# Kernel tuning notes

Measured on AMD Instinct MI355X. Metric: run time of the kernel, lower is better.

The kernel has to match this reference:

```python
import jax, jax.numpy as jnp
import numpy as np

# Dimensions: B batches, E links, T time steps, F flows, rank-r factors, K unrolled iters
B, E, T, F = 16, 256, 4096, 512
RANK = 10
NUM_ITER = 5


def setup_inputs() -> dict:
    key = jax.random.key(0)
    ks = jax.random.split(key, 9)
    Y = jax.random.normal(ks[0], (B, E, T), dtype=jnp.float32)
    R = (jax.random.uniform(ks[1], (B, E, F)) < 0.1).astype(jnp.float32)
    Omega = (jax.random.uniform(ks[2], (B, E, T)) < 0.9).astype(jnp.float32)
    P0 = jax.random.normal(ks[3], (B, E, RANK), dtype=jnp.float32) * 0.1
    Q0 = jax.random.normal(ks[4], (B, T, RANK), dtype=jnp.float32) * 0.1
    # per-iteration learned log-parameters of the unrolled network
    lam_log = jax.random.normal(ks[5], (NUM_ITER,), dtype=jnp.float32) * 0.1 - 1.0
    mu_log = jax.random.normal(ks[6], (NUM_ITER,), dtype=jnp.float32) * 0.1 - 1.0
    nu_log = jax.random.normal(ks[7], (NUM_ITER,), dtype=jnp.float32) * 0.1
    gamma_logit = jax.random.normal(ks[8], (NUM_ITER,), dtype=jnp.float32) * 0.1
    return {"Y": Y, "R": R, "Omega": Omega, "P0": P0, "Q0": Q0,
            "lam_log": lam_log, "mu_log": mu_log, "nu_log": nu_log,
            "gamma_logit": gamma_logit}


def reference(Y, R, Omega, P0, Q0, lam_log, mu_log, nu_log, gamma_logit):
    """Unrolled BSCA: Y ~ X + R @ A + noise on observed entries (Omega mask),
    X relaxed low-rank via factors P (B,E,r), Q (B,T,r); A sparse anomalies (B,F,T).
    Each iteration: rank-r ridge solves for P and Q (left=False -> rhs @ inv(lhs)),
    relaxed X update, soft-thresholded BSCA direction for A + convex-combination step."""
    rank = P0.shape[-1]
    eye = jnp.eye(rank, dtype=Y.dtype)
    X = Omega * Y                     # (B,E,T) init relaxed variable
    A = jnp.zeros((*Y.shape[:-2], R.shape[-1], Y.shape[-1]), dtype=Y.dtype)  # (B,F,T)
    P, Q = P0, Q0
    A_scale = (R * R).mT @ (Omega * Omega)          # (B,F,T)
    noobs = A_scale == 0
    A_scale_safe = A_scale + noobs.astype(Y.dtype)
    for k in range(NUM_ITER):
        lam = jnp.exp(lam_log[k])
        mu = jnp.exp(mu_log[k])
        nu = jnp.exp(nu_log[k])
        gamma = jax.nn.sigmoid(gamma_logit[k])
        regp = lam / nu
        # P update: P = (X @ Q) @ inv(Q^T Q + regp I)   (right solve; lhs symmetric)
        lhsQ = Q.mT @ Q + regp * eye                 # (B,r,r)
        P = jnp.linalg.solve(lhsQ, (X @ Q).mT).mT    # (B,E,r)
        # Q update: Q = (X^T @ P) @ inv(P^T P + regp I)
        lhsP = P.mT @ P + regp * eye
        Q = jnp.linalg.solve(lhsP, (X.mT @ P).mT).mT # (B,T,r)
        # X update (relaxed): X = (Omega*err + nu*P Q^T) / (Omega^2 + nu)
        RA = R @ A                                   # (B,E,T)
        err = Omega * (Y - RA)
        X = (Omega * err + nu * (P @ Q.mT)) / (Omega * Omega + nu)
        # A update: soft-thresholded best-response + convex combination step
        resid = Omega * (Y - X - RA)                 # (B,E,T)
        BA = A + (R.mT @ resid) / A_scale_safe       # (B,F,T)
        A_dir = jnp.sign(BA) * jnp.maximum(jnp.abs(BA) - mu / A_scale_safe, 0.0)
        A_dir = jnp.where(noobs, 0.0, A_dir)
        A = A + gamma * (A_dir - A)
    return A
```

## Files before the change

### kernel.cpp

```cpp
#include <hip/hip_runtime.h>
#include <stdint.h>

#define BB 16
#define EE 256
#define TT 4096
#define FF 512
#define RK 10
#define NIT 5

typedef short bf16x8 __attribute__((ext_vector_type(8)));
typedef float f32x4  __attribute__((ext_vector_type(4)));

__device__ __forceinline__ unsigned short f2bf(float x){
  unsigned int u = __float_as_uint(x);
  unsigned int r = (u + 0x7FFFu + ((u >> 16) & 1u)) >> 16;
  return (unsigned short)r;
}
__device__ __forceinline__ float bf2f(unsigned short s){
  return __uint_as_float(((unsigned int)s) << 16);
}

__device__ __forceinline__ void gld16(const void* g, void* l){
  __builtin_amdgcn_global_load_lds((const __attribute__((address_space(1))) unsigned int*)g,
                                   (__attribute__((address_space(3))) unsigned int*)l,
                                   16, 0, 0);
}

__device__ __forceinline__ int ssw(int r, int s){
  return ((s ^ (r & 3) ^ ((r >> 2) & 3)) << 3);
}


__global__ void k_params(const float* lam_log, const float* mu_log,
                         const float* nu_log, const float* gl, float* prm){
  int k = threadIdx.x;
  if (k < NIT){
    float lam = expf(lam_log[k]);
    float mu  = expf(mu_log[k]);
    float nu  = expf(nu_log[k]);
    float gam = 1.0f/(1.0f+expf(-gl[k]));
    prm[k*8+0]=lam; prm[k*8+1]=mu; prm[k*8+2]=nu; prm[k*8+3]=gam; prm[k*8+4]=lam/nu;
  }
}

__global__ void k_initX(const float4* __restrict__ Y, const float4* __restrict__ Om,
                        float4* __restrict__ X, ushort4* __restrict__ Omb){
  int i = blockIdx.x*256 + threadIdx.x;
  float4 y = Y[i], o = Om[i];
  X[i] = make_float4(y.x*o.x, y.y*o.y, y.z*o.z, y.w*o.w);
  ushort4 ob; ob.x=f2bf(o.x); ob.y=f2bf(o.y); ob.z=f2bf(o.z); ob.w=f2bf(o.w);
  Omb[i] = ob;
}

__global__ void k_qtrans(const float* __restrict__ Q0, float* __restrict__ Qt){
  int idx = blockIdx.x*256 + threadIdx.x;
  int b = idx >> 12, t = idx & (TT-1);
  #pragma unroll
  for (int j=0;j<RK;j++)
    Qt[((size_t)b*RK + j)*TT + t] = Q0[(size_t)idx*RK + j];
}

__global__ void k_rbf(const float4* __restrict__ R, ushort4* __restrict__ Rb){
  int i = blockIdx.x*256 + threadIdx.x;
  float4 v = R[i];
  ushort4 o; o.x=f2bf(v.x); o.y=f2bf(v.y); o.z=f2bf(v.z); o.w=f2bf(v.w);
  Rb[i] = o;
}

__global__ void k_rtransb(const float* __restrict__ Rm, unsigned short* __restrict__ Rbt){
  int f = blockIdx.x, b = blockIdx.y, e = threadIdx.x;
  Rbt[((size_t)b*FF + f)*EE + e] = f2bf(Rm[((size_t)b*EE + e)*FF + f]);
}

__global__ void k_omtrans(const unsigned short* __restrict__ Omb,
                          unsigned short* __restrict__ OmbT){
  __shared__ unsigned short sT[64][66];
  int b  = blockIdx.z;
  int E0 = blockIdx.y*64, T0 = blockIdx.x*64;
  int tid = threadIdx.x;
  int fi = tid >> 4;
  int m  = tid & 15;
  #pragma unroll
  for (int pass=0; pass<4; ++pass){
    int e = pass*16 + fi;
    ushort4 v = *(const ushort4*)(Omb + ((size_t)(b*EE + E0 + e))*TT + T0 + m*4);
    sT[e][m*4+0]=v.x; sT[e][m*4+1]=v.y; sT[e][m*4+2]=v.z; sT[e][m*4+3]=v.w;
  }
  __syncthreads();
  #pragma unroll
  for (int pass=0; pass<4; ++pass){
    int t  = pass*16 + fi;
    int e4 = m*4;
    ushort4 o;
    o.x = sT[e4+0][t]; o.y = sT[e4+1][t];
    o.z = sT[e4+2][t]; o.w = sT[e4+3][t];
    *(ushort4*)(OmbT + ((size_t)b*TT + T0 + t)*EE + E0 + e4) = o;
  }
}


__global__ void k_lhsQ(const float* __restrict__ Qt, const float* __restrict__ prm,
                       float* __restrict__ lhs, int k){
  int p = blockIdx.x, b = blockIdx.y;
  int i = 0, rem = p;
  while (rem >= i+1){ rem -= (i+1); ++i; }
  int j = rem;
  const float* qi = Qt + ((size_t)b*RK + i)*TT;
  const float* qj = Qt + ((size_t)b*RK + j)*TT;
  float a = 0.0f;
  for (int t = threadIdx.x*4; t < TT; t += 1024){
    float4 x = *(const float4*)(qi+t);
    float4 y = *(const float4*)(qj+t);
    a += x.x*y.x + x.y*y.y + x.z*y.z + x.w*y.w;
  }
  __shared__ float red[256];
  red[threadIdx.x] = a; __syncthreads();
  for (int s=128; s>0; s>>=1){
    if (threadIdx.x < s) red[threadIdx.x] += red[threadIdx.x+s];
    __syncthreads();
  }
  if (threadIdx.x==0){
    float v = red[0];
    if (i==j) v += prm[k*8+4];
    lhs[(b*RK+i)*RK + j] = v;
    lhs[(b*RK+j)*RK + i] = v;
  }
}

__global__ void k_lhsP(const float* __restrict__ P, const float* __restrict__ prm,
                       float* __restrict__ lhs, int k){
  int p = blockIdx.x, b = blockIdx.y;
  int i = 0, rem = p;
  while (rem >= i+1){ rem -= (i+1); ++i; }
  int j = rem;
  int e = threadIdx.x;
  const float* pr = P + ((size_t)b*EE + e)*RK;
  float a = pr[i]*pr[j];
  __shared__ float red[256];
  red[threadIdx.x] = a; __syncthreads();
  for (int s=128; s>0; s>>=1){
    if (threadIdx.x < s) red[threadIdx.x] += red[threadIdx.x+s];
    __syncthreads();
  }
  if (threadIdx.x==0){
    float v = red[0];
    if (i==j) v += prm[k*8+4];
    lhs[(b*RK+i)*RK + j] = v;
    lhs[(b*RK+j)*RK + i] = v;
  }
}

__global__ void k_invert(const float* __restrict__ lhs, float* __restrict__ inv){
  int b = blockIdx.x;
  __shared__ float aug[RK][2*RK];
  int tid = threadIdx.x;
  int i = tid / (2*RK), j = tid % (2*RK);
  bool act = tid < RK*2*RK;
  if (act) aug[i][j] = (j < RK) ? lhs[(b*RK+i)*RK + j] : ((j-RK)==i ? 1.0f : 0.0f);
  __syncthreads();
  for (int kk=0; kk<RK; ++kk){
    float pinv = 1.0f / aug[kk][kk];
    __syncthreads();
    if (act && i==kk) aug[i][j] *= pinv;
    __syncthreads();
    float factor = (act && i!=kk) ? aug[i][kk] : 0.0f;
    float pivrow = act ? aug[kk][j] : 0.0f;
    __syncthreads();
    if (act && i!=kk) aug[i][j] -= factor * pivrow;
    __syncthreads();
  }
  if (act && j >= RK) inv[(b*RK+i)*RK + (j-RK)] = aug[i][j];
}

__global__ void k_Pupd(const float* __restrict__ X, const float* __restrict__ Qt,
                       const float* __restrict__ inv, float* __restrict__ P){
  int e = blockIdx.x, b = blockIdx.y;
  const float* xr = X + ((size_t)b*EE + e)*TT;
  const float* qb = Qt + (size_t)b*RK*TT;
  float acc[RK];
  #pragma unroll
  for (int j=0;j<RK;j++) acc[j]=0.0f;
  for (int t = threadIdx.x*4; t < TT; t += 1024){
    float4 x = *(const float4*)(xr+t);
    #pragma unroll
    for (int j=0;j<RK;j++){
      float4 q = *(const float4*)(qb + (size_t)j*TT + t);
      acc[j] += x.x*q.x + x.y*q.y + x.z*q.z + x.w*q.w;
    }
  }
  __shared__ float partial[4][RK];
  int lane = threadIdx.x & 63, wv = threadIdx.x >> 6;
  #pragma unroll
  for (int j=0;j<RK;j++){
    float v = acc[j];
    for (int s=32;s>0;s>>=1) v += __shfl_down(v, s, 64);
    if (lane==0) partial[wv][j] = v;
  }
  __syncthreads();
  if (threadIdx.x < RK){
    int i = threadIdx.x;
    float out = 0.0f;
    #pragma unroll
    for (int j=0;j<RK;j++){
      float xq = partial[0][j]+partial[1][j]+partial[2][j]+partial[3][j];
      out += xq * inv[(b*RK+j)*RK + i];
    }
    P[((size_t)b*EE + e)*RK + i] = out;
  }
}

__global__ void k_Qupd(const float* __restrict__ X, const float* __restrict__ P,
                       const float* __restrict__ inv, float* __restrict__ Qt){
  int b = blockIdx.y;
  int t = blockIdx.x*256 + threadIdx.x;
  __shared__ float sP[EE*RK];
  __shared__ float sInv[RK*RK];
  for (int i=threadIdx.x; i<EE*RK; i+=256) sP[i] = P[(size_t)b*EE*RK + i];
  if (threadIdx.x < RK*RK) sInv[threadIdx.x] = inv[b*RK*RK + threadIdx.x];
  __syncthreads();
  float acc[RK];
  #pragma unroll
  for (int j=0;j<RK;j++) acc[j]=0.0f;
  const float* xb = X + (size_t)b*EE*TT + t;
  for (int e=0;e<EE;e++){
    float x = xb[(size_t)e*TT];
    #pragma unroll
    for (int j=0;j<RK;j++) acc[j] += x * sP[e*RK+j];
  }
  #pragma unroll
  for (int i=0;i<RK;i++){
    float q = 0.0f;
    #pragma unroll
    for (int j=0;j<RK;j++) q += acc[j]*sInv[j*RK+i];
    Qt[((size_t)b*RK + i)*TT + t] = q;
  }
}

__global__ __launch_bounds__(256) void k_gemm1m(
    const unsigned short* __restrict__ Abt, const unsigned short* __restrict__ Rb,
    const float* __restrict__ Y, const unsigned short* __restrict__ Omb,
    const float* __restrict__ Qt, const float* __restrict__ P,
    const float* __restrict__ prm, float* __restrict__ X,
    unsigned short* __restrict__ residT, int k)
{
  __shared__ __align__(16) unsigned char lds[20480];
  int id = blockIdx.x;
  int b  = id >> 6;
  int e0 = ((id >> 5) & 1) * 128;
  int t0 = (id & 31) * 128;
  int tid  = threadIdx.x;
  int lane = tid & 63, wid = tid >> 6;
  int lr = lane & 15, lg = lane >> 4;
  int wm = wid >> 1, wn = wid & 1;

  f32x4 acc[4][4];
  #pragma unroll
  for (int m=0;m<4;++m)
    #pragma unroll
    for (int n=0;n<4;++n)
      #pragma unroll
      for (int i=0;i<4;++i) acc[m][n][i]=0.0f;

  if (k > 0){
    int swz  = ((lg ^ (lr & 3) ^ ((lr >> 2) & 3)) << 4);
    int aoff = (wm*64 + lr)*64 + swz;
    int boff = 8192 + (wn*64 + lr)*64 + swz;
    int c0 = tid, c1 = tid + 256;
    int r0 = c0 >> 2, s0 = c0 & 3;
    int r1 = c1 >> 2, s1 = c1 & 3;
    const unsigned short* gA0 = Abt + ((size_t)b*TT + t0 + r0)*FF + ssw(r0,s0);
    const unsigned short* gA1 = Abt + ((size_t)b*TT + t0 + r1)*FF + ssw(r1,s1);
    const unsigned short* gB0 = Rb  + ((size_t)(b*EE + e0 + r0))*FF + ssw(r0,s0);
    const unsigned short* gB1 = Rb  + ((size_t)(b*EE + e0 + r1))*FF + ssw(r1,s1);
    unsigned char* lA0 = lds + c0*16;
    unsigned char* lA1 = lds + c1*16;
    unsigned char* lB0 = lds + 8192 + c0*16;
    unsigned char* lB1 = lds + 8192 + c1*16;

    for (int kk=0; kk<16; ++kk){
      __syncthreads();
      int f0k = kk*32;
      gld16(gA0 + f0k, lA0);
      gld16(gA1 + f0k, lA1);
      gld16(gB0 + f0k, lB0);
      gld16(gB1 + f0k, lB1);
      asm volatile("s_waitcnt vmcnt(0)" ::: "memory");
      __syncthreads();
      bf16x8 af[4], bb[4];
      #pragma unroll
      for (int m=0;m<4;++m) af[m] = *(const bf16x8*)(lds + aoff + m*1024);
      #pragma unroll
      for (int n=0;n<4;++n) bb[n] = *(const bf16x8*)(lds + boff + n*1024);
      #pragma unroll
      for (int m=0;m<4;++m)
        #pragma unroll
        for (int n=0;n<4;++n)
          acc[m][n] = __builtin_amdgcn_mfma_f32_16x16x32_bf16(af[m], bb[n], acc[m][n], 0, 0, 0);
    }
  }

  __syncthreads();
  unsigned short* wbuf = (unsigned short*)(lds + wid*2176);
  float* Pl = (float*)(lds + 8704);
  float* Ql = (float*)(lds + 8704 + 5120);
  for (int idx = tid; idx < 128*RK; idx += 256)
    Pl[idx] = P[((size_t)(b*EE + e0))*RK + idx];
  for (int idx = tid; idx < RK*128; idx += 256){
    int j = idx >> 7, t = idx & 127;
    Ql[idx] = Qt[((size_t)(b*RK + j))*TT + t0 + t];
  }
  __syncthreads();

  float nu = prm[k*8+2];
  #pragma unroll
  for (int m=0;m<4;++m){
    int tq = wm*64 + m*16 + lg*4;
    float4 ql4[RK];
    #pragma unroll
    for (int j=0;j<RK;++j) ql4[j] = *(const float4*)(Ql + j*128 + tq);
    asm volatile("" ::: "memory");
    #pragma unroll
    for (int n=0;n<4;++n){
      int eloc = wn*64 + n*16 + lr;
      const float* pr = Pl + eloc*RK;
      float4 pq = {0,0,0,0};
      #pragma unroll
      for (int j=0;j<RK;++j){
        float pj = pr[j];
        pq.x += pj*ql4[j].x; pq.y += pj*ql4[j].y;
        pq.z += pj*ql4[j].z; pq.w += pj*ql4[j].w;
      }
      f32x4 ra = acc[m][n];
      size_t off = ((size_t)(b*EE + e0 + eloc))*TT + t0 + tq;
      float4 y = *(const float4*)(Y + off);
      ushort4 ou = *(const ushort4*)(Omb + off);
      float4 xo; float rs0, rs1, rs2, rs3;
      {
        float o = bf2f(ou.x), om2 = o*o, d = y.x - ra[0];
        xo.x = (om2*d + nu*pq.x)/(om2 + nu); rs0 = o*(y.x - xo.x - ra[0]);
      }{
        float o = bf2f(ou.y), om2 = o*o, d = y.y - ra[1];
        xo.y = (om2*d + nu*pq.y)/(om2 + nu); rs1 = o*(y.y - xo.y - ra[1]);
      }{
        float o = bf2f(ou.z), om2 = o*o, d = y.z - ra[2];
        xo.z = (om2*d + nu*pq.z)/(om2 + nu); rs2 = o*(y.z - xo.z - ra[2]);
      }{
        float o = bf2f(ou.w), om2 = o*o, d = y.w - ra[3];
        xo.w = (om2*d + nu*pq.w)/(om2 + nu); rs3 = o*(y.w - xo.w - ra[3]);
      }
      *(float4*)(X + off) = xo;
      int wc = n*16 + lr;
      wbuf[(lg*4+0)*68 + wc] = f2bf(rs0);
      wbuf[(lg*4+1)*68 + wc] = f2bf(rs1);
      wbuf[(lg*4+2)*68 + wc] = f2bf(rs2);
      wbuf[(lg*4+3)*68 + wc] = f2bf(rs3);
    }
    asm volatile("" ::: "memory");
    #pragma unroll
    for (int j2=0;j2<4;++j2){
      int row = j2*4 + lg;
      int c4  = lr*4;
      ushort4 vv = *(const ushort4*)(wbuf + row*68 + c4);
      *(ushort4*)(residT + ((size_t)b*TT + t0 + wm*64 + m*16 + row)*EE + e0 + wn*64 + c4) = vv;
    }
    asm volatile("" ::: "memory");
  }
}

__device__ __forceinline__ float aupd(float a, float g, unsigned short asu,
                                      float mu, float gamma){
  float as = bf2f(asu);
  bool no = (as == 0.0f);
  float rs = 1.0f / (no ? 1.0f : as);
  float ba = a + g*rs;
  float ad = copysignf(fmaxf(fabsf(ba) - mu*rs, 0.0f), ba);
  if (no) ad = 0.0f;
  return a + gamma*(ad - a);
}

__global__ __launch_bounds__(256) void k_gemm2m(
    const unsigned short* __restrict__ residT, const unsigned short* __restrict__ Rbt,
    const unsigned short* __restrict__ As, const float* __restrict__ prm,
    float* __restrict__ A, unsigned short* __restrict__ Abt, int k)
{
  __shared__ __align__(16) unsigned char lds[16384];
  int id = blockIdx.x;
  int b  = id >> 7;
  int f0 = ((id >> 5) & 3) * 128;
  int t0 = (id & 31) * 128;
  int tid  = threadIdx.x;
  int lane = tid & 63, wid = tid >> 6;
  int lr = lane & 15, lg = lane >> 4;
  int wm = wid >> 1, wn = wid & 1;

  f32x4 acc[4][4];
  #pragma unroll
  for (int m=0;m<4;++m)
    #pragma unroll
    for (int n=0;n<4;++n)
      #pragma unroll
      for (int i=0;i<4;++i) acc[m][n][i]=0.0f;

  int swz  = ((lg ^ (lr & 3) ^ ((lr >> 2) & 3)) << 4);
  int aoff = (wm*64 + lr)*64 + swz;
  int boff = 8192 + (wn*64 + lr)*64 + swz;
  int c0 = tid, c1 = tid + 256;
  int r0 = c0 >> 2, s0 = c0 & 3;
  int r1 = c1 >> 2, s1 = c1 & 3;
  const unsigned short* gA0 = residT + ((size_t)b*TT + t0 + r0)*EE + ssw(r0,s0);
  const unsigned short* gA1 = residT + ((size_t)b*TT + t0 + r1)*EE + ssw(r1,s1);
  const unsigned short* gB0 = Rbt    + ((size_t)(b*FF + f0 + r0))*EE + ssw(r0,s0);
  const unsigned short* gB1 = Rbt    + ((size_t)(b*FF + f0 + r1))*EE + ssw(r1,s1);
  unsigned char* lA0 = lds + c0*16;
  unsigned char* lA1 = lds + c1*16;
  unsigned char* lB0 = lds + 8192 + c0*16;
  unsigned char* lB1 = lds + 8192 + c1*16;

  for (int kk=0; kk<8; ++kk){
    __syncthreads();
    int eoff = kk*32;
    gld16(gA0 + eoff, lA0);
    gld16(gA1 + eoff, lA1);
    gld16(gB0 + eoff, lB0);
    gld16(gB1 + eoff, lB1);
    asm volatile("s_waitcnt vmcnt(0)" ::: "memory");
    __syncthreads();
    bf16x8 af[4], bb[4];
    #pragma unroll
    for (int m=0;m<4;++m) af[m] = *(const bf16x8*)(lds + aoff + m*1024);
    #pragma unroll
    for (int n=0;n<4;++n) bb[n] = *(const bf16x8*)(lds + boff + n*1024);
    #pragma unroll
    for (int m=0;m<4;++m)
      #pragma unroll
      for (int n=0;n<4;++n)
        acc[m][n] = __builtin_amdgcn_mfma_f32_16x16x32_bf16(af[m], bb[n], acc[m][n], 0, 0, 0);
  }

  __syncthreads();
  unsigned short* wbuf = (unsigned short*)(lds + wid*2176);
  float mu = prm[k*8+1], gamma = prm[k*8+3];
  bool emit = (k < NIT-1);
  #pragma unroll
  for (int m=0;m<4;++m){
    int tq = wm*64 + m*16 + lg*4;
    #pragma unroll
    for (int n=0;n<4;++n){
      int floc = wn*64 + n*16 + lr;
      size_t off = ((size_t)(b*FF + f0 + floc))*TT + t0 + tq;
      float4 a = *(const float4*)(A + off);
      ushort4 as4 = *(const ushort4*)(As + off);
      f32x4 g = acc[m][n];
      float4 an;
      an.x = aupd(a.x, g[0], as4.x, mu, gamma);
      an.y = aupd(a.y, g[1], as4.y, mu, gamma);
      an.z = aupd(a.z, g[2], as4.z, mu, gamma);
      an.w = aupd(a.w, g[3], as4.w, mu, gamma);
      *(float4*)(A + off) = an;
      if (emit){
        int wc = n*16 + lr;
        wbuf[(lg*4+0)*68 + wc] = f2bf(an.x);
        wbuf[(lg*4+1)*68 + wc] = f2bf(an.y);
        wbuf[(lg*4+2)*68 + wc] = f2bf(an.z);
        wbuf[(lg*4+3)*68 + wc] = f2bf(an.w);
      }
    }
    asm volatile("" ::: "memory");
    if (emit){
      #pragma unroll
      for (int j2=0;j2<4;++j2){
        int row = j2*4 + lg;
        int c4  = lr*4;
        ushort4 vv = *(const ushort4*)(wbuf + row*68 + c4);
        *(ushort4*)(Abt + ((size_t)b*TT + t0 + wm*64 + m*16 + row)*FF + f0 + wn*64 + c4) = vv;
      }
    }
    asm volatile("" ::: "memory");
  }
}

__global__ __launch_bounds__(256) void k_ascalem(
    const unsigned short* __restrict__ OmbT, const unsigned short* __restrict__ Rbt,
    unsigned short* __restrict__ As)
{
  __shared__ __align__(16) unsigned char lds[16384];
  int id = blockIdx.x;
  int b  = id >> 7;
  int f0 = ((id >> 5) & 3) * 128;
  int t0 = (id & 31) * 128;
  int tid  = threadIdx.x;
  int lane = tid & 63, wid = tid >> 6;
  int lr = lane & 15, lg = lane >> 4;
  int wm = wid >> 1, wn = wid & 1;

  f32x4 acc[4][4];
  #pragma unroll
  for (int m=0;m<4;++m)
    #pragma unroll
    for (int n=0;n<4;++n)
      #pragma unroll
      for (int i=0;i<4;++i) acc[m][n][i]=0.0f;

  int swz  = ((lg ^ (lr & 3) ^ ((lr >> 2) & 3)) << 4);
  int aoff = (wm*64 + lr)*64 + swz;
  int boff = 8192 + (wn*64 + lr)*64 + swz;
  int c0 = tid, c1 = tid + 256;
  int r0 = c0 >> 2, s0 = c0 & 3;
  int r1 = c1 >> 2, s1 = c1 & 3;
  const unsigned short* gA0 = OmbT + ((size_t)b*TT + t0 + r0)*EE + ssw(r0,s0);
  const unsigned short* gA1 = OmbT + ((size_t)b*TT + t0 + r1)*EE + ssw(r1,s1);
  const unsigned short* gB0 = Rbt  + ((size_t)(b*FF + f0 + r0))*EE + ssw(r0,s0);
  const unsigned short* gB1 = Rbt  + ((size_t)(b*FF + f0 + r1))*EE + ssw(r1,s1);
  unsigned char* lA0 = lds + c0*16;
  unsigned char* lA1 = lds + c1*16;
  unsigned char* lB0 = lds + 8192 + c0*16;
  unsigned char* lB1 = lds + 8192 + c1*16;

  for (int kk=0; kk<8; ++kk){
    __syncthreads();
    int eoff = kk*32;
    gld16(gA0 + eoff, lA0);
    gld16(gA1 + eoff, lA1);
    gld16(gB0 + eoff, lB0);
    gld16(gB1 + eoff, lB1);
    asm volatile("s_waitcnt vmcnt(0)" ::: "memory");
    __syncthreads();
    bf16x8 af[4], bb[4];
    #pragma unroll
    for (int m=0;m<4;++m) af[m] = *(const bf16x8*)(lds + aoff + m*1024);
    #pragma unroll
    for (int n=0;n<4;++n) bb[n] = *(const bf16x8*)(lds + boff + n*1024);
    #pragma unroll
    for (int m=0;m<4;++m)
      #pragma unroll
      for (int n=0;n<4;++n)
        acc[m][n] = __builtin_amdgcn_mfma_f32_16x16x32_bf16(af[m], bb[n], acc[m][n], 0, 0, 0);
  }

  #pragma unroll
  for (int m=0;m<4;++m){
    int tq = wm*64 + m*16 + lg*4;
    #pragma unroll
    for (int n=0;n<4;++n){
      int floc = wn*64 + n*16 + lr;
      size_t off = ((size_t)(b*FF + f0 + floc))*TT + t0 + tq;
      ushort4 o;
      o.x = f2bf(acc[m][n][0]); o.y = f2bf(acc[m][n][1]);
      o.z = f2bf(acc[m][n][2]); o.w = f2bf(acc[m][n][3]);
      *(ushort4*)(As + off) = o;
    }
  }
}


extern "C" void kernel_launch(void* const* d_in, const int* in_sizes, int n_in,
                              void* d_out, int out_size, void* d_ws, size_t ws_size,
                              hipStream_t stream){
  const float* Y   = (const float*)d_in[0];
  const float* Rm  = (const float*)d_in[1];
  const float* Om  = (const float*)d_in[2];
  const float* P0  = (const float*)d_in[3];
  const float* Q0  = (const float*)d_in[4];
  const float* lam = (const float*)d_in[5];
  const float* mu  = (const float*)d_in[6];
  const float* nu  = (const float*)d_in[7];
  const float* gl  = (const float*)d_in[8];
  float* A = (float*)d_out;

  char* ws = (char*)d_ws;
  const size_t X_OFF    = 0;
  const size_t REST_OFF = X_OFF    + (size_t)BB*EE*TT*4;
  const size_t OMB_OFF  = REST_OFF + (size_t)BB*TT*EE*2;
  const size_t AS_OFF   = OMB_OFF  + (size_t)BB*EE*TT*2;
  const size_t QT_OFF   = AS_OFF   + (size_t)BB*FF*TT*2;
  const size_t P_OFF    = QT_OFF   + (size_t)BB*RK*TT*4;
  const size_t LHS_OFF  = P_OFF    + (size_t)BB*EE*RK*4;
  const size_t INV_OFF  = LHS_OFF  + (size_t)BB*RK*RK*4;
  const size_t PRM_OFF  = INV_OFF  + (size_t)BB*RK*RK*4;
  const size_t RB_OFF   = PRM_OFF  + 4096;
  const size_t RBT_OFF  = RB_OFF   + (size_t)BB*EE*FF*2;
  const size_t OMBT_OFF = RBT_OFF  + (size_t)BB*FF*EE*2;
  const size_t ABT_OFF  = OMBT_OFF + (size_t)BB*TT*EE*2;

  float* X    = (float*)(ws + X_OFF);
  unsigned short* residT = (unsigned short*)(ws + REST_OFF);
  unsigned short* Omb    = (unsigned short*)(ws + OMB_OFF);
  unsigned short* As     = (unsigned short*)(ws + AS_OFF);
  float* Qt   = (float*)(ws + QT_OFF);
  float* P    = (float*)(ws + P_OFF);
  float* lhs  = (float*)(ws + LHS_OFF);
  float* inv  = (float*)(ws + INV_OFF);
  float* prm  = (float*)(ws + PRM_OFF);
  unsigned short* Rb   = (unsigned short*)(ws + RB_OFF);
  unsigned short* Rbt  = (unsigned short*)(ws + RBT_OFF);
  unsigned short* OmbT = (unsigned short*)(ws + OMBT_OFF);
  unsigned short* Abt  = (unsigned short*)(ws + ABT_OFF);

  (void)P0; (void)Om; (void)in_sizes; (void)n_in; (void)ws_size;

  hipMemsetAsync(d_out, 0, (size_t)out_size*sizeof(float), stream);
  k_params<<<1, 64, 0, stream>>>(lam, mu, nu, gl, prm);
  k_initX<<<BB*EE*TT/4/256, 256, 0, stream>>>((const float4*)Y, (const float4*)Om,
                                              (float4*)X, (ushort4*)Omb);
  k_qtrans<<<BB*TT/256, 256, 0, stream>>>(Q0, Qt);
  k_rbf<<<BB*EE*FF/4/256, 256, 0, stream>>>((const float4*)Rm, (ushort4*)Rb);
  k_rtransb<<<dim3(FF, BB), 256, 0, stream>>>(Rm, Rbt);
  k_omtrans<<<dim3(TT/64, EE/64, BB), 256, 0, stream>>>(Omb, OmbT);
  k_ascalem<<<2048, 256, 0, stream>>>(OmbT, Rbt, As);

  for (int k=0; k<NIT; ++k){
    k_lhsQ  <<<dim3(55, BB), 256, 0, stream>>>(Qt, prm, lhs, k);
    k_invert<<<BB, 256, 0, stream>>>(lhs, inv);
    k_Pupd  <<<dim3(EE, BB), 256, 0, stream>>>(X, Qt, inv, P);
    k_lhsP  <<<dim3(55, BB), 256, 0, stream>>>(P, prm, lhs, k);
    k_invert<<<BB, 256, 0, stream>>>(lhs, inv);
    k_Qupd  <<<dim3(TT/256, BB), 256, 0, stream>>>(X, P, inv, Qt);
    k_gemm1m<<<BB*2*32, 256, 0, stream>>>(Abt, Rb, Y, Omb, Qt, P, prm, X, residT, k);
    k_gemm2m<<<2048, 256, 0, stream>>>(residT, Rbt, As, prm, A, Abt, k);
  }
}
```

Measured before the change: 1.797 ms.

## Halve GEMM tile sizes for more blocks and pack Omega into bitmask

The two per-iteration MFMA GEMM kernels get smaller output tiles: gemm1m goes to 64x128 and 2048 blocks, gemm2m to 128x64 and 4096 blocks. This raises block count and lowers per-block registers and LDS to improve occupancy and load balance across CUs. Separately, a new kernel packs the binary Omega mask into 32-bit bitmasks with wave ballots, so gemm1m reads one bit per element instead of a bf16 value. The bitmask relies on Omega being binary. Smaller tiles mean more redundant operand loads per output.

```diff
diff --git a/kernel.cpp b/kernel.cpp
--- a/kernel.cpp
+++ b/kernel.cpp
@@ -50,6 +50,18 @@
   X[i] = make_float4(y.x*o.x, y.y*o.y, y.z*o.z, y.w*o.w);
   ushort4 ob; ob.x=f2bf(o.x); ob.y=f2bf(o.y); ob.z=f2bf(o.z); ob.w=f2bf(o.w);
   Omb[i] = ob;
+}
+
+__global__ void k_ombit(const float* __restrict__ Om, unsigned int* __restrict__ Ombit){
+  int tid = threadIdx.x;
+  int wv = tid >> 6, lane = tid & 63;
+  size_t base = (size_t)blockIdx.x*8192 + (size_t)wv*2048;
+  for (int it=0; it<32; ++it){
+    float om = Om[base + it*64 + lane];
+    unsigned long long m = __ballot(om != 0.0f);
+    if (lane==0)  Ombit[(base>>5) + it*2]     = (unsigned int)m;
+    if (lane==32) Ombit[(base>>5) + it*2 + 1] = (unsigned int)(m>>32);
+  }
 }
 
 __global__ void k_qtrans(const float* __restrict__ Q0, float* __restrict__ Qt){
@@ -238,24 +250,24 @@
 
 __global__ __launch_bounds__(256) void k_gemm1m(
     const unsigned short* __restrict__ Abt, const unsigned short* __restrict__ Rb,
-    const float* __restrict__ Y, const unsigned short* __restrict__ Omb,
+    const float* __restrict__ Y, const unsigned int* __restrict__ Ombit,
     const float* __restrict__ Qt, const float* __restrict__ P,
     const float* __restrict__ prm, float* __restrict__ X,
     unsigned short* __restrict__ residT, int k)
 {
   __shared__ __align__(16) unsigned char lds[20480];
   int id = blockIdx.x;
-  int b  = id >> 6;
-  int e0 = ((id >> 5) & 1) * 128;
-  int t0 = (id & 31) * 128;
+  int b  = id >> 7;
+  int e0 = ((id >> 6) & 1) * 128;
+  int t0 = (id & 63) * 64;
   int tid  = threadIdx.x;
   int lane = tid & 63, wid = tid >> 6;
   int lr = lane & 15, lg = lane >> 4;
   int wm = wid >> 1, wn = wid & 1;
 
-  f32x4 acc[4][4];
-  #pragma unroll
-  for (int m=0;m<4;++m)
+  f32x4 acc[2][4];
+  #pragma unroll
+  for (int m=0;m<2;++m)
     #pragma unroll
     for (int n=0;n<4;++n)
       #pragma unroll
@@ -263,36 +275,34 @@
 
   if (k > 0){
     int swz  = ((lg ^ (lr & 3) ^ ((lr >> 2) & 3)) << 4);
-    int aoff = (wm*64 + lr)*64 + swz;
-    int boff = 8192 + (wn*64 + lr)*64 + swz;
+    int aoff = (wm*32 + lr)*64 + swz;
+    int boff = 4096 + (wn*64 + lr)*64 + swz;
+    int rA = tid >> 2, sA = tid & 3;
     int c0 = tid, c1 = tid + 256;
-    int r0 = c0 >> 2, s0 = c0 & 3;
-    int r1 = c1 >> 2, s1 = c1 & 3;
-    const unsigned short* gA0 = Abt + ((size_t)b*TT + t0 + r0)*FF + ssw(r0,s0);
-    const unsigned short* gA1 = Abt + ((size_t)b*TT + t0 + r1)*FF + ssw(r1,s1);
-    const unsigned short* gB0 = Rb  + ((size_t)(b*EE + e0 + r0))*FF + ssw(r0,s0);
-    const unsigned short* gB1 = Rb  + ((size_t)(b*EE + e0 + r1))*FF + ssw(r1,s1);
-    unsigned char* lA0 = lds + c0*16;
-    unsigned char* lA1 = lds + c1*16;
-    unsigned char* lB0 = lds + 8192 + c0*16;
-    unsigned char* lB1 = lds + 8192 + c1*16;
+    int rB0 = c0 >> 2, sB0 = c0 & 3;
+    int rB1 = c1 >> 2, sB1 = c1 & 3;
+    const unsigned short* gA  = Abt + ((size_t)b*TT + t0 + rA)*FF + ssw(rA,sA);
+    const unsigned short* gB0 = Rb  + ((size_t)(b*EE + e0 + rB0))*FF + ssw(rB0,sB0);
+    const unsigned short* gB1 = Rb  + ((size_t)(b*EE + e0 + rB1))*FF + ssw(rB1,sB1);
+    unsigned char* lA  = lds + tid*16;
+    unsigned char* lB0 = lds + 4096 + c0*16;
+    unsigned char* lB1 = lds + 4096 + c1*16;
 
     for (int kk=0; kk<16; ++kk){
       __syncthreads();
       int f0k = kk*32;
-      gld16(gA0 + f0k, lA0);
-      gld16(gA1 + f0k, lA1);
+      gld16(gA  + f0k, lA);
       gld16(gB0 + f0k, lB0);
       gld16(gB1 + f0k, lB1);
       asm volatile("s_waitcnt vmcnt(0)" ::: "memory");
       __syncthreads();
-      bf16x8 af[4], bb[4];
-      #pragma unroll
-      for (int m=0;m<4;++m) af[m] = *(const bf16x8*)(lds + aoff + m*1024);
+      bf16x8 af[2], bb[4];
+      #pragma unroll
+      for (int m=0;m<2;++m) af[m] = *(const bf16x8*)(lds + aoff + m*1024);
       #pragma unroll
       for (int n=0;n<4;++n) bb[n] = *(const bf16x8*)(lds + boff + n*1024);
       #pragma unroll
-      for (int m=0;m<4;++m)
+      for (int m=0;m<2;++m)
         #pragma unroll
         for (int n=0;n<4;++n)
           acc[m][n] = __builtin_amdgcn_mfma_f32_16x16x32_bf16(af[m], bb[n], acc[m][n], 0, 0, 0);
@@ -301,23 +311,23 @@
 
   __syncthreads();
   unsigned short* wbuf = (unsigned short*)(lds + wid*2176);
-  float* Pl = (float*)(lds + 8704);
-  float* Ql = (float*)(lds + 8704 + 5120);
+  float* Pl = (float*)(lds + 12288);
+  float* Ql = (float*)(lds + 12288 + 5120);
   for (int idx = tid; idx < 128*RK; idx += 256)
     Pl[idx] = P[((size_t)(b*EE + e0))*RK + idx];
-  for (int idx = tid; idx < RK*128; idx += 256){
-    int j = idx >> 7, t = idx & 127;
+  for (int idx = tid; idx < RK*64; idx += 256){
+    int j = idx >> 6, t = idx & 63;
     Ql[idx] = Qt[((size_t)(b*RK + j))*TT + t0 + t];
   }
   __syncthreads();
 
   float nu = prm[k*8+2];
   #pragma unroll
-  for (int m=0;m<4;++m){
-    int tq = wm*64 + m*16 + lg*4;
+  for (int m=0;m<2;++m){
+    int tq = wm*32 + m*16 + lg*4;
     float4 ql4[RK];
     #pragma unroll
-    for (int j=0;j<RK;++j) ql4[j] = *(const float4*)(Ql + j*128 + tq);
+    for (int j=0;j<RK;++j) ql4[j] = *(const float4*)(Ql + j*64 + tq);
     asm volatile("" ::: "memory");
     #pragma unroll
     for (int n=0;n<4;++n){
@@ -333,20 +343,21 @@
       f32x4 ra = acc[m][n];
       size_t off = ((size_t)(b*EE + e0 + eloc))*TT + t0 + tq;
       float4 y = *(const float4*)(Y + off);
-      ushort4 ou = *(const ushort4*)(Omb + off);
+      unsigned int w = Ombit[off >> 5];
+      int sh = (int)(off & 31);
       float4 xo; float rs0, rs1, rs2, rs3;
       {
-        float o = bf2f(ou.x), om2 = o*o, d = y.x - ra[0];
-        xo.x = (om2*d + nu*pq.x)/(om2 + nu); rs0 = o*(y.x - xo.x - ra[0]);
+        float om2 = (w>>(sh+0))&1 ? 1.0f : 0.0f; float d = y.x - ra[0];
+        xo.x = (om2*d + nu*pq.x)/(om2 + nu); rs0 = om2*(y.x - xo.x - ra[0]);
       }{
-        float o = bf2f(ou.y), om2 = o*o, d = y.y - ra[1];
-        xo.y = (om2*d + nu*pq.y)/(om2 + nu); rs1 = o*(y.y - xo.y - ra[1]);
+        float om2 = (w>>(sh+1))&1 ? 1.0f : 0.0f; float d = y.y - ra[1];
+        xo.y = (om2*d + nu*pq.y)/(om2 + nu); rs1 = om2*(y.y - xo.y - ra[1]);
       }{
-        float o = bf2f(ou.z), om2 = o*o, d = y.z - ra[2];
-        xo.z = (om2*d + nu*pq.z)/(om2 + nu); rs2 = o*(y.z - xo.z - ra[2]);
+        float om2 = (w>>(sh+2))&1 ? 1.0f : 0.0f; float d = y.z - ra[2];
+        xo.z = (om2*d + nu*pq.z)/(om2 + nu); rs2 = om2*(y.z - xo.z - ra[2]);
       }{
-        float o = bf2f(ou.w), om2 = o*o, d = y.w - ra[3];
-        xo.w = (om2*d + nu*pq.w)/(om2 + nu); rs3 = o*(y.w - xo.w - ra[3]);
+        float om2 = (w>>(sh+3))&1 ? 1.0f : 0.0f; float d = y.w - ra[3];
+        xo.w = (om2*d + nu*pq.w)/(om2 + nu); rs3 = om2*(y.w - xo.w - ra[3]);
       }
       *(float4*)(X + off) = xo;
       int wc = n*16 + lr;
@@ -361,7 +372,7 @@
       int row = j2*4 + lg;
       int c4  = lr*4;
       ushort4 vv = *(const ushort4*)(wbuf + row*68 + c4);
-      *(ushort4*)(residT + ((size_t)b*TT + t0 + wm*64 + m*16 + row)*EE + e0 + wn*64 + c4) = vv;
+      *(ushort4*)(residT + ((size_t)b*TT + t0 + wm*32 + m*16 + row)*EE + e0 + wn*64 + c4) = vv;
     }
     asm volatile("" ::: "memory");
   }
@@ -383,70 +394,68 @@
     const unsigned short* __restrict__ As, const float* __restrict__ prm,
     float* __restrict__ A, unsigned short* __restrict__ Abt, int k)
 {
-  __shared__ __align__(16) unsigned char lds[16384];
+  __shared__ __align__(16) unsigned char lds[12288];
   int id = blockIdx.x;
-  int b  = id >> 7;
-  int f0 = ((id >> 5) & 3) * 128;
+  int b  = id >> 8;
+  int f0 = ((id >> 5) & 7) * 64;
   int t0 = (id & 31) * 128;
   int tid  = threadIdx.x;
   int lane = tid & 63, wid = tid >> 6;
   int lr = lane & 15, lg = lane >> 4;
   int wm = wid >> 1, wn = wid & 1;
 
-  f32x4 acc[4][4];
+  f32x4 acc[4][2];
   #pragma unroll
   for (int m=0;m<4;++m)
     #pragma unroll
-    for (int n=0;n<4;++n)
+    for (int n=0;n<2;++n)
       #pragma unroll
       for (int i=0;i<4;++i) acc[m][n][i]=0.0f;
 
   int swz  = ((lg ^ (lr & 3) ^ ((lr >> 2) & 3)) << 4);
   int aoff = (wm*64 + lr)*64 + swz;
-  int boff = 8192 + (wn*64 + lr)*64 + swz;
+  int boff = 8192 + (wn*32 + lr)*64 + swz;
   int c0 = tid, c1 = tid + 256;
   int r0 = c0 >> 2, s0 = c0 & 3;
   int r1 = c1 >> 2, s1 = c1 & 3;
+  int rB = tid >> 2, sB = tid & 3;
   const unsigned short* gA0 = residT + ((size_t)b*TT + t0 + r0)*EE + ssw(r0,s0);
   const unsigned short* gA1 = residT + ((size_t)b*TT + t0 + r1)*EE + ssw(r1,s1);
-  const unsigned short* gB0 = Rbt    + ((size_t)(b*FF + f0 + r0))*EE + ssw(r0,s0);
-  const unsigned short* gB1 = Rbt    + ((size_t)(b*FF + f0 + r1))*EE + ssw(r1,s1);
+  const unsigned short* gB  = Rbt    + ((size_t)(b*FF + f0 + rB))*EE + ssw(rB,sB);
   unsigned char* lA0 = lds + c0*16;
   unsigned char* lA1 = lds + c1*16;
-  unsigned char* lB0 = lds + 8192 + c0*16;
-  unsigned char* lB1 = lds + 8192 + c1*16;
+  unsigned char* lB  = lds + 8192 + tid*16;
 
   for (int kk=0; kk<8; ++kk){
     __syncthreads();
     int eoff = kk*32;
     gld16(gA0 + eoff, lA0);
     gld16(gA1 + eoff, lA1);
-    gld16(gB0 + eoff, lB0);
-    gld16(gB1 + eoff, lB1);
+    gld16(gB  + eoff, lB);
     asm volatile("s_waitcnt vmcnt(0)" ::: "memory");
     __syncthreads();
-    bf16x8 af[4], bb[4];
+    bf16x8 af[4], bb[2];
     #pragma unroll
     for (int m=0;m<4;++m) af[m] = *(const bf16x8*)(lds + aoff + m*1024);
     #pragma unroll
-    for (int n=0;n<4;++n) bb[n] = *(const bf16x8*)(lds + boff + n*1024);
+    for (int n=0;n<2;++n) bb[n] = *(const bf16x8*)(lds + boff + n*1024);
     #pragma unroll
     for (int m=0;m<4;++m)
       #pragma unroll
-      for (int n=0;n<4;++n)
+      for (int n=0;n<2;++n)
         acc[m][n] = __builtin_amdgcn_mfma_f32_16x16x32_bf16(af[m], bb[n], acc[m][n], 0, 0, 0);
   }
 
   __syncthreads();
-  unsigned short* wbuf = (unsigned short*)(lds + wid*2176);
+  unsigned short* wbuf = (unsigned short*)(lds + wid*1152);
   float mu = prm[k*8+1], gamma = prm[k*8+3];
   bool emit = (k < NIT-1);
   #pragma unroll
   for (int m=0;m<4;++m){
     int tq = wm*64 + m*16 + lg*4;
     #pragma unroll
-    for (int n=0;n<4;++n){
-      int floc = wn*64 + n*16 + lr;
+    for (int n=0;n<2;++n){
+      int floc = wn*32 + n*16 + lr;
       size_t off = ((size_t)(b*FF + f0 + floc))*TT + t0 + tq;
       float4 a = *(const float4*)(A + off);
       ushort4 as4 = *(const ushort4*)(As + off);
@@ -459,20 +468,20 @@
       *(float4*)(A + off) = an;
       if (emit){
         int wc = n*16 + lr;
-        wbuf[(lg*4+0)*68 + wc] = f2bf(an.x);
-        wbuf[(lg*4+1)*68 + wc] = f2bf(an.y);
-        wbuf[(lg*4+2)*68 + wc] = f2bf(an.z);
-        wbuf[(lg*4+3)*68 + wc] = f2bf(an.w);
+        wbuf[(lg*4+0)*36 + wc] = f2bf(an.x);
+        wbuf[(lg*4+1)*36 + wc] = f2bf(an.y);
+        wbuf[(lg*4+2)*36 + wc] = f2bf(an.z);
+        wbuf[(lg*4+3)*36 + wc] = f2bf(an.w);
       }
     }
     asm volatile("" ::: "memory");
     if (emit){
       #pragma unroll
-      for (int j2=0;j2<4;++j2){
-        int row = j2*4 + lg;
-        int c4  = lr*4;
-        ushort4 vv = *(const ushort4*)(wbuf + row*68 + c4);
-        *(ushort4*)(Abt + ((size_t)b*TT + t0 + wm*64 + m*16 + row)*FF + f0 + wn*64 + c4) = vv;
+      for (int j2=0;j2<2;++j2){
+        int row = j2*8 + (lane >> 3);
+        int c4  = (lane & 7)*4;
+        ushort4 vv = *(const ushort4*)(wbuf + row*36 + c4);
+        *(ushort4*)(Abt + ((size_t)b*TT + t0 + wm*64 + m*16 + row)*FF + f0 + wn*32 + c4) = vv;
       }
     }
     asm volatile("" ::: "memory");
@@ -581,6 +590,7 @@
   const size_t RBT_OFF  = RB_OFF   + (size_t)BB*EE*FF*2;
   const size_t OMBT_OFF = RBT_OFF  + (size_t)BB*FF*EE*2;
   const size_t ABT_OFF  = OMBT_OFF + (size_t)BB*TT*EE*2;
+  const size_t OBIT_OFF = ABT_OFF  + (size_t)BB*TT*FF*2;
 
   float* X    = (float*)(ws + X_OFF);
   unsigned short* residT = (unsigned short*)(ws + REST_OFF);
@@ -591,17 +601,19 @@
   float* lhs  = (float*)(ws + LHS_OFF);
   float* inv  = (float*)(ws + INV_OFF);
   float* prm  = (float*)(ws + PRM_OFF);
-  unsigned short* Rb   = (unsigned short*)(ws + RB_OFF);
-  unsigned short* Rbt  = (unsigned short*)(ws + RBT_OFF);
-  unsigned short* OmbT = (unsigned short*)(ws + OMBT_OFF);
-  unsigned short* Abt  = (unsigned short*)(ws + ABT_OFF);
-
-  (void)P0; (void)Om; (void)in_sizes; (void)n_in; (void)ws_size;
+  unsigned short* Rb    = (unsigned short*)(ws + RB_OFF);
+  unsigned short* Rbt   = (unsigned short*)(ws + RBT_OFF);
+  unsigned short* OmbT  = (unsigned short*)(ws + OMBT_OFF);
+  unsigned short* Abt   = (unsigned short*)(ws + ABT_OFF);
+  unsigned int*   Ombit = (unsigned int*)(ws + OBIT_OFF);
+
+  (void)P0; (void)in_sizes; (void)n_in; (void)ws_size;
 
   hipMemsetAsync(d_out, 0, (size_t)out_size*sizeof(float), stream);
   k_params<<<1, 64, 0, stream>>>(lam, mu, nu, gl, prm);
   k_initX<<<BB*EE*TT/4/256, 256, 0, stream>>>((const float4*)Y, (const float4*)Om,
                                               (float4*)X, (ushort4*)Omb);
+  k_ombit<<<BB*EE*TT/8192, 256, 0, stream>>>(Om, Ombit);
   k_qtrans<<<BB*TT/256, 256, 0, stream>>>(Q0, Qt);
   k_rbf<<<BB*EE*FF/4/256, 256, 0, stream>>>((const float4*)Rm, (ushort4*)Rb);
   k_rtransb<<<dim3(FF, BB), 256, 0, stream>>>(Rm, Rbt);
@@ -615,7 +627,7 @@
     k_lhsP  <<<dim3(55, BB), 256, 0, stream>>>(P, prm, lhs, k);
     k_invert<<<BB, 256, 0, stream>>>(lhs, inv);
     k_Qupd  <<<dim3(TT/256, BB), 256, 0, stream>>>(X, P, inv, Qt);
-    k_gemm1m<<<BB*2*32, 256, 0, stream>>>(Abt, Rb, Y, Omb, Qt, P, prm, X, residT, k);
-    k_gemm2m<<<2048, 256, 0, stream>>>(residT, Rbt, As, prm, A, Abt, k);
-  }
-}
+    k_gemm1m<<<2048, 256, 0, stream>>>(Abt, Rb, Y, Ombit, Qt, P, prm, X, residT, k);
+    k_gemm2m<<<4096, 256, 0, stream>>>(residT, Rbt, As, prm, A, Abt, k);
+  }
+}
```

New measurement: 1.806 ms. About the same (+0.5%).
